# Kernel tuning notes

Hardware: AMD Instinct MI355X
Metric: run time of the kernel (lower is better)

Reference implementation:

```python
import jax, jax.numpy as jnp
import numpy as np

DELTA = 5.0          # weight on positive BCE term
R = 0.01             # hard-negative fraction
M, N = 4096, 16384   # batch rows, memory-bank size
NUM_HARD = int(R * (N - 1))  # int(r * neg_count); each row has exactly 1 positive


def setup_inputs() -> dict:
    key = jax.random.key(0)
    k1, k2 = jax.random.split(key)
    inputs = jax.random.normal(k1, (M, N), dtype=jnp.float32)
    targets = jax.random.randint(k2, (M,), 0, N)
    return {"inputs": inputs, "targets": targets}


def reference(inputs, targets):
    m, n = inputs.shape
    rows = jnp.arange(m)
    # positive logit per row (one-hot scatter => exactly one positive)
    pos = inputs[rows, targets]                          # [m]
    # BCE with logits, target=1: softplus(-x); mean over the single positive
    l_pos = jax.nn.softplus(-pos)                        # [m]
    # exclude positive from negatives by sinking it to -inf, then hard top-k
    neg_inf = jnp.finfo(inputs.dtype).min
    masked = inputs.at[rows, targets].set(neg_inf)       # [m, n]
    hard_neg, _ = jax.lax.top_k(masked, NUM_HARD)        # [m, NUM_HARD]
    # BCE with logits, target=0: softplus(x); mean over hard negatives
    l_neg = jnp.mean(jax.nn.softplus(hard_neg), axis=1)  # [m]
    return jnp.mean(DELTA * l_pos + l_neg)
```

## Files before the change

### kernel.cpp

```cpp
#include <hip/hip_runtime.h>
#include <stdint.h>

#define M_ROWS 4096
#define N_COLS 16384
#define K_HARD 163
#define DELTA_W 5.0f
#define CAPW   256
#define NWAVE  4
#define CAP    (CAPW * NWAVE)
#define NB     1024
#define BLOCK  256

#define KEY_MIN  0xC0000000u
#define BIN_BIAS 3072

__device__ __forceinline__ uint32_t f2key(float x) {
    uint32_t u = __float_as_uint(x);
    return u ^ (uint32_t)(((int32_t)u >> 31) | 0x80000000u);
}
__device__ __forceinline__ float key2f(uint32_t k) {
    uint32_t u = (k & 0x80000000u) ? (k & 0x7fffffffu) : ~k;
    return __uint_as_float(u);
}
__device__ __forceinline__ float softplus_f(float x) {
    return fmaxf(x, 0.0f) + log1pf(__expf(-fabsf(x)));
}

__device__ void pivot_scan(const uint32_t* hist, int K,
                           int* part, int* pivot, int* krem) {
    const int t = threadIdx.x;
    const int bpt = NB / BLOCK;
    const int base = t * bpt;
    int mypart = 0;
    for (int i = 0; i < bpt; ++i) mypart += (int)hist[base + i];
    part[t] = mypart;
    __syncthreads();
    for (int off = 1; off < BLOCK; off <<= 1) {
        int v = part[t];
        if (t + off < BLOCK) v += part[t + off];
        __syncthreads();
        part[t] = v;
        __syncthreads();
    }
    const int above = part[t] - mypart;
    if (above < K && above + mypart >= K) {
        int running = above;
        for (int b = base + bpt - 1; b >= base; --b) {
            int c = (int)hist[b];
            if (running < K && running + c >= K) { *pivot = b; *krem = K - running; }
            running += c;
        }
    }
    __syncthreads();
}

__global__ __launch_bounds__(BLOCK) void mmcl_kernel(
        const float* __restrict__ inputs,
        const int* __restrict__ targets,
        float* __restrict__ out) {
    __shared__ uint32_t s_hist[NB];
    __shared__ uint32_t s_cand[CAP];
    __shared__ uint32_t s_cand2[CAP];
    __shared__ int s_part[BLOCK];
    __shared__ int s_cnt[NWAVE];
    __shared__ int s_found;
    __shared__ int s_pivot;
    __shared__ int s_krem;
    __shared__ float s_wsum[NWAVE];

    const int row = blockIdx.x;
    const int t = threadIdx.x;
    const int lane = t & 63;
    const int wid = t >> 6;
    const float* rowp = inputs + (size_t)row * N_COLS;
    const int target = targets[row];

    for (int i = t; i < NB; i += BLOCK) s_hist[i] = 0;
    if (t == 0) s_found = -1;

    uint32_t* wcand = s_cand + wid * CAPW;
    int wcount = 0;
    const float4* rp4 = (const float4*)rowp;
#pragma unroll 4
    for (int it = 0; it < N_COLS / (BLOCK * 4); ++it) {
        const float4 v = rp4[it * BLOCK + t];
        const float vals[4] = {v.x, v.y, v.z, v.w};
#pragma unroll
        for (int c = 0; c < 4; ++c) {
            const uint32_t k = f2key(vals[c]);
            const bool pred = (k >= KEY_MIN);
            const unsigned long long mask = __ballot(pred);
            if (pred) {
                const int below = __builtin_amdgcn_mbcnt_hi(
                    (uint32_t)(mask >> 32),
                    __builtin_amdgcn_mbcnt_lo((uint32_t)mask, 0));
                const int off = wcount + below;
                if (off < CAPW) wcand[off] = k;
            }
            wcount += (int)__popcll(mask);
        }
    }
    if (lane == 0) s_cnt[wid] = wcount;
    __syncthreads();

    const int c0 = s_cnt[0], c1 = s_cnt[1], c2 = s_cnt[2], c3 = s_cnt[3];
    const int total = c0 + c1 + c2 + c3;
    const bool no_ovf = (c0 <= CAPW) & (c1 <= CAPW) & (c2 <= CAPW) & (c3 <= CAPW);
    const int wbase = (wid > 0 ? c0 : 0) + (wid > 1 ? c1 : 0) + (wid > 2 ? c2 : 0);

    const float pos = rowp[target];
    const uint32_t tkey = f2key(pos);

    if (no_ovf) {
        const int mycnt = s_cnt[wid];
        for (int i = lane; i < mycnt; i += 64) s_cand2[wbase + i] = wcand[i];
    }
    __syncthreads();

    if (no_ovf && tkey >= KEY_MIN) {
        for (int i = t; i < total; i += BLOCK)
            if (s_cand2[i] == tkey) { atomicCAS(&s_found, -1, i); break; }
    }
    __syncthreads();
    int ncand = total;
    if (s_found >= 0) {
        if (t == 0) s_cand2[s_found] = s_cand2[total - 1];
        ncand = total - 1;
    }
    __syncthreads();
    const bool fast = no_ovf && (ncand >= K_HARD);

    float local = 0.0f;
    uint32_t T;
    int tie;

    if (fast) {
        for (int i = t; i < ncand; i += BLOCK)
            atomicAdd(&s_hist[(s_cand2[i] >> 20) - BIN_BIAS], 1u);
        __syncthreads();
        pivot_scan(s_hist, K_HARD, s_part, &s_pivot, &s_krem);
        const int p1b = s_pivot + BIN_BIAS, k1r = s_krem;

        for (int i = t; i < NB; i += BLOCK) s_hist[i] = 0;
        __syncthreads();
        for (int i = t; i < ncand; i += BLOCK) {
            const uint32_t k = s_cand2[i];
            if ((int)(k >> 20) == p1b) atomicAdd(&s_hist[(k >> 10) & 1023u], 1u);
        }
        __syncthreads();
        pivot_scan(s_hist, k1r, s_part, &s_pivot, &s_krem);
        const int p2 = s_pivot, k2r = s_krem;
        const uint32_t pref2 = ((uint32_t)p1b << 10) | (uint32_t)p2;

        for (int i = t; i < NB; i += BLOCK) s_hist[i] = 0;
        __syncthreads();
        for (int i = t; i < ncand; i += BLOCK) {
            const uint32_t k = s_cand2[i];
            if ((k >> 10) == pref2) atomicAdd(&s_hist[k & 1023u], 1u);
        }
        __syncthreads();
        pivot_scan(s_hist, k2r, s_part, &s_pivot, &s_krem);
        T = (pref2 << 10) | (uint32_t)s_pivot;
        tie = s_krem;

        for (int i = t; i < ncand; i += BLOCK) {
            const uint32_t k = s_cand2[i];
            if (k > T) local += softplus_f(key2f(k));
        }
    } else {
        for (int i = t; i < NB; i += BLOCK) s_hist[i] = 0;
        __syncthreads();
        for (int j = t; j < N_COLS; j += BLOCK) {
            if (j == target) continue;
            atomicAdd(&s_hist[f2key(rowp[j]) >> 22], 1u);
        }
        __syncthreads();
        pivot_scan(s_hist, K_HARD, s_part, &s_pivot, &s_krem);
        const int p1 = s_pivot, k1r = s_krem;

        for (int i = t; i < NB; i += BLOCK) s_hist[i] = 0;
        __syncthreads();
        for (int j = t; j < N_COLS; j += BLOCK) {
            if (j == target) continue;
            const uint32_t k = f2key(rowp[j]);
            if ((int)(k >> 22) == p1) atomicAdd(&s_hist[(k >> 12) & 1023u], 1u);
        }
        __syncthreads();
        pivot_scan(s_hist, k1r, s_part, &s_pivot, &s_krem);
        const uint32_t pref2 = ((uint32_t)p1 << 10) | (uint32_t)s_pivot;
        const int k2r = s_krem;

        for (int i = t; i < NB; i += BLOCK) s_hist[i] = 0;
        __syncthreads();
        for (int j = t; j < N_COLS; j += BLOCK) {
            if (j == target) continue;
            const uint32_t k = f2key(rowp[j]);
            if ((k >> 12) == pref2) atomicAdd(&s_hist[(k >> 2) & 1023u], 1u);
        }
        __syncthreads();
        pivot_scan(s_hist, k2r, s_part, &s_pivot, &s_krem);
        const uint32_t pref3 = (pref2 << 10) | (uint32_t)s_pivot;
        const int k3r = s_krem;

        for (int i = t; i < NB; i += BLOCK) s_hist[i] = 0;
        __syncthreads();
        for (int j = t; j < N_COLS; j += BLOCK) {
            if (j == target) continue;
            const uint32_t k = f2key(rowp[j]);
            if ((k >> 2) == pref3) atomicAdd(&s_hist[k & 3u], 1u);
        }
        __syncthreads();
        if (t == 0) {
            int running = 0;
            for (int b = 3; b >= 0; --b) {
                const int c = (int)s_hist[b];
                if (running < k3r && running + c >= k3r) {
                    s_pivot = b; s_krem = k3r - running;
                }
                running += c;
            }
        }
        __syncthreads();
        T = (pref3 << 2) | (uint32_t)s_pivot;
        tie = s_krem;

        for (int j = t; j < N_COLS; j += BLOCK) {
            if (j == target) continue;
            const uint32_t k = f2key(rowp[j]);
            if (k > T) local += softplus_f(key2f(k));
        }
    }

    for (int off = 32; off > 0; off >>= 1) local += __shfl_down(local, off);
    if (lane == 0) s_wsum[wid] = local;
    __syncthreads();
    if (t == 0) {
        float tot = 0.0f;
        for (int w = 0; w < NWAVE; ++w) tot += s_wsum[w];
        tot += (float)tie * softplus_f(key2f(T));
        const float l_neg = tot / (float)K_HARD;
        const float l_pos = softplus_f(-pos);
        const float rowval = (DELTA_W * l_pos + l_neg) * (1.0f / (float)M_ROWS);
        atomicAdd(out, rowval);
    }
}

__global__ void mmcl_zero_out(float* out) { out[0] = 0.0f; }

extern "C" void kernel_launch(void* const* d_in, const int* in_sizes, int n_in,
                              void* d_out, int out_size, void* d_ws, size_t ws_size,
                              hipStream_t stream) {
    const float* inputs = (const float*)d_in[0];
    const int* targets = (const int*)d_in[1];
    float* out = (float*)d_out;
    mmcl_zero_out<<<1, 1, 0, stream>>>(out);
    mmcl_kernel<<<M_ROWS, BLOCK, 0, stream>>>(inputs, targets, out);
}
```

Baseline: 382.5 us.

## Replace ballot compaction and three-pass radix select with per-thread slots and one-pass histogram

Candidate collection drops the per-element wave ballot and compaction. Each thread now writes values at or above 2.0 into private shared-memory slots without branching, and a prefix scan compacts them into one array. Top-k selection replaces three histogram-plus-pivot passes with one 1024-bin histogram over the candidate range, a shuffle-based suffix scan, and an exact rank sort of the pivot bin's few elements. This cuts barriers and LDS atomics per row, at the cost of more shared memory, which may lower occupancy, and a full-row fallback when slots or the small buffer overflow.

```diff
diff --git a/kernel.cpp b/kernel.cpp
--- a/kernel.cpp
+++ b/kernel.cpp
@@ -5,14 +5,13 @@
 #define N_COLS 16384
 #define K_HARD 163
 #define DELTA_W 5.0f
-#define CAPW   256
-#define NWAVE  4
-#define CAP    (CAPW * NWAVE)
+#define BLOCK  256
+#define SLOTS  12
+#define CAP    1024
 #define NB     1024
-#define BLOCK  256
-
-#define KEY_MIN  0xC0000000u
-#define BIN_BIAS 3072
+#define SMALL  64
+#define THRESH 2.0f
+#define KEY_MIN 0xC0000000u
 
 __device__ __forceinline__ uint32_t f2key(float x) {
     uint32_t u = __float_as_uint(x);
@@ -58,15 +57,13 @@
         const float* __restrict__ inputs,
         const int* __restrict__ targets,
         float* __restrict__ out) {
-    __shared__ uint32_t s_hist[NB];
+    __shared__ float    s_slots_f[BLOCK * SLOTS];
     __shared__ uint32_t s_cand[CAP];
-    __shared__ uint32_t s_cand2[CAP];
-    __shared__ int s_part[BLOCK];
-    __shared__ int s_cnt[NWAVE];
-    __shared__ int s_found;
-    __shared__ int s_pivot;
-    __shared__ int s_krem;
-    __shared__ float s_wsum[NWAVE];
+    __shared__ int s_wt[4], s_wm[4];
+    __shared__ int s_found, s_pivot, s_krem, s_nsmall;
+    __shared__ uint32_t s_skey[SMALL];
+    __shared__ int s_sidx[SMALL];
+    __shared__ float s_fw[4];
 
     const int row = blockIdx.x;
     const int t = threadIdx.x;
@@ -75,145 +72,174 @@
     const float* rowp = inputs + (size_t)row * N_COLS;
     const int target = targets[row];
 
-    for (int i = t; i < NB; i += BLOCK) s_hist[i] = 0;
     if (t == 0) s_found = -1;
 
-    uint32_t* wcand = s_cand + wid * CAPW;
-    int wcount = 0;
+    float* myslots = s_slots_f + t * SLOTS;
+    uint32_t cnt = 0;
     const float4* rp4 = (const float4*)rowp;
 #pragma unroll 4
     for (int it = 0; it < N_COLS / (BLOCK * 4); ++it) {
         const float4 v = rp4[it * BLOCK + t];
-        const float vals[4] = {v.x, v.y, v.z, v.w};
-#pragma unroll
-        for (int c = 0; c < 4; ++c) {
-            const uint32_t k = f2key(vals[c]);
-            const bool pred = (k >= KEY_MIN);
-            const unsigned long long mask = __ballot(pred);
-            if (pred) {
-                const int below = __builtin_amdgcn_mbcnt_hi(
-                    (uint32_t)(mask >> 32),
-                    __builtin_amdgcn_mbcnt_lo((uint32_t)mask, 0));
-                const int off = wcount + below;
-                if (off < CAPW) wcand[off] = k;
-            }
-            wcount += (int)__popcll(mask);
-        }
-    }
-    if (lane == 0) s_cnt[wid] = wcount;
-    __syncthreads();
-
-    const int c0 = s_cnt[0], c1 = s_cnt[1], c2 = s_cnt[2], c3 = s_cnt[3];
-    const int total = c0 + c1 + c2 + c3;
-    const bool no_ovf = (c0 <= CAPW) & (c1 <= CAPW) & (c2 <= CAPW) & (c3 <= CAPW);
-    const int wbase = (wid > 0 ? c0 : 0) + (wid > 1 ? c1 : 0) + (wid > 2 ? c2 : 0);
+        myslots[min(cnt, (uint32_t)(SLOTS - 1))] = v.x; cnt += (v.x >= THRESH);
+        myslots[min(cnt, (uint32_t)(SLOTS - 1))] = v.y; cnt += (v.y >= THRESH);
+        myslots[min(cnt, (uint32_t)(SLOTS - 1))] = v.z; cnt += (v.z >= THRESH);
+        myslots[min(cnt, (uint32_t)(SLOTS - 1))] = v.w; cnt += (v.w >= THRESH);
+    }
+
+    const int stored = (int)min(cnt, (uint32_t)SLOTS);
+    int inc = stored;
+    for (int off = 1; off < 64; off <<= 1) {
+        int y = __shfl_up(inc, off);
+        if (lane >= off) inc += y;
+    }
+    int mx = (int)cnt;
+    for (int off = 1; off < 64; off <<= 1)
+        mx = max(mx, __shfl_xor(mx, off));
+    if (lane == 63) { s_wt[wid] = inc; }
+    if (lane == 0)  { s_wm[wid] = mx; }
+    __syncthreads();
+    const int w0 = s_wt[0], w1 = s_wt[1], w2 = s_wt[2], w3 = s_wt[3];
+    const int total = w0 + w1 + w2 + w3;
+    const int maxc = max(max(s_wm[0], s_wm[1]), max(s_wm[2], s_wm[3]));
+    const int wbase = (wid > 0 ? w0 : 0) + (wid > 1 ? w1 : 0) + (wid > 2 ? w2 : 0);
+    const int myoff = wbase + inc - stored;
+    for (int c = 0; c < stored; ++c) {
+        const int d = myoff + c;
+        if (d < CAP) s_cand[d] = f2key(myslots[c]);
+    }
+    __syncthreads();
 
     const float pos = rowp[target];
     const uint32_t tkey = f2key(pos);
-
-    if (no_ovf) {
-        const int mycnt = s_cnt[wid];
-        for (int i = lane; i < mycnt; i += 64) s_cand2[wbase + i] = wcand[i];
-    }
-    __syncthreads();
-
-    if (no_ovf && tkey >= KEY_MIN) {
-        for (int i = t; i < total; i += BLOCK)
-            if (s_cand2[i] == tkey) { atomicCAS(&s_found, -1, i); break; }
+    const int tclamp = min(total, CAP);
+    if (pos >= THRESH) {
+        for (int i = t; i < tclamp; i += BLOCK)
+            if (s_cand[i] == tkey) { atomicCAS(&s_found, -1, i); break; }
     }
     __syncthreads();
     int ncand = total;
     if (s_found >= 0) {
-        if (t == 0) s_cand2[s_found] = s_cand2[total - 1];
         ncand = total - 1;
-    }
-    __syncthreads();
-    const bool fast = no_ovf && (ncand >= K_HARD);
-
+        if (t == 0) s_cand[s_found] = s_cand[ncand];
+    }
+    __syncthreads();
+
+    const bool fast = (maxc <= SLOTS) && (total <= CAP) && (ncand >= K_HARD);
+    bool needfb = !fast;
     float local = 0.0f;
-    uint32_t T;
-    int tie;
+
+    uint32_t* hist = (uint32_t*)s_slots_f;
 
     if (fast) {
+        for (int i = t; i < NB; i += BLOCK) hist[i] = 0;
+        __syncthreads();
         for (int i = t; i < ncand; i += BLOCK)
-            atomicAdd(&s_hist[(s_cand2[i] >> 20) - BIN_BIAS], 1u);
-        __syncthreads();
-        pivot_scan(s_hist, K_HARD, s_part, &s_pivot, &s_krem);
-        const int p1b = s_pivot + BIN_BIAS, k1r = s_krem;
-
-        for (int i = t; i < NB; i += BLOCK) s_hist[i] = 0;
-        __syncthreads();
+            atomicAdd(&hist[min((s_cand[i] - KEY_MIN) >> 14, (uint32_t)(NB - 1))], 1u);
+        __syncthreads();
+
+        const int base4 = t * 4;
+        const int c0 = (int)hist[base4], c1 = (int)hist[base4 + 1],
+                  c2 = (int)hist[base4 + 2], c3 = (int)hist[base4 + 3];
+        const int own = c0 + c1 + c2 + c3;
+        int suf = own;
+        for (int off = 1; off < 64; off <<= 1) {
+            int y = __shfl_down(suf, off);
+            if (lane + off < 64) suf += y;
+        }
+        if (lane == 0) s_wt[wid] = suf;
+        if (t == 0) s_nsmall = 0;
+        __syncthreads();
+        int wsuf = 0;
+        for (int w = wid + 1; w < 4; ++w) wsuf += s_wt[w];
+        int run = wsuf + (suf - own);
+        {
+            const int cs[4] = {c0, c1, c2, c3};
+            for (int b = 3; b >= 0; --b) {
+                const int c = cs[b];
+                if (run < K_HARD && run + c >= K_HARD) {
+                    s_pivot = base4 + b; s_krem = K_HARD - run;
+                }
+                run += c;
+            }
+        }
+        __syncthreads();
+        const uint32_t B = (uint32_t)s_pivot;
+        const int krem = s_krem;
+
         for (int i = t; i < ncand; i += BLOCK) {
-            const uint32_t k = s_cand2[i];
-            if ((int)(k >> 20) == p1b) atomicAdd(&s_hist[(k >> 10) & 1023u], 1u);
-        }
-        __syncthreads();
-        pivot_scan(s_hist, k1r, s_part, &s_pivot, &s_krem);
-        const int p2 = s_pivot, k2r = s_krem;
-        const uint32_t pref2 = ((uint32_t)p1b << 10) | (uint32_t)p2;
-
-        for (int i = t; i < NB; i += BLOCK) s_hist[i] = 0;
-        __syncthreads();
-        for (int i = t; i < ncand; i += BLOCK) {
-            const uint32_t k = s_cand2[i];
-            if ((k >> 10) == pref2) atomicAdd(&s_hist[k & 1023u], 1u);
-        }
-        __syncthreads();
-        pivot_scan(s_hist, k2r, s_part, &s_pivot, &s_krem);
-        T = (pref2 << 10) | (uint32_t)s_pivot;
-        tie = s_krem;
-
-        for (int i = t; i < ncand; i += BLOCK) {
-            const uint32_t k = s_cand2[i];
-            if (k > T) local += softplus_f(key2f(k));
-        }
-    } else {
-        for (int i = t; i < NB; i += BLOCK) s_hist[i] = 0;
-        __syncthreads();
-        for (int j = t; j < N_COLS; j += BLOCK) {
-            if (j == target) continue;
-            atomicAdd(&s_hist[f2key(rowp[j]) >> 22], 1u);
-        }
-        __syncthreads();
-        pivot_scan(s_hist, K_HARD, s_part, &s_pivot, &s_krem);
+            const uint32_t k = s_cand[i];
+            const uint32_t kb = min((k - KEY_MIN) >> 14, (uint32_t)(NB - 1));
+            if (kb > B) local += softplus_f(key2f(k));
+            else if (kb == B) {
+                const int d = atomicAdd(&s_nsmall, 1);
+                if (d < SMALL) { s_skey[d] = k; s_sidx[d] = i; }
+            }
+        }
+        __syncthreads();
+        const int m = s_nsmall;
+        if (m > SMALL) { needfb = true; local = 0.0f; }
+        else {
+            for (int i = t; i < m; i += BLOCK) {
+                const uint32_t ki = s_skey[i]; const int ii = s_sidx[i];
+                int r = 0;
+                for (int j = 0; j < m; ++j) {
+                    const uint32_t kj = s_skey[j];
+                    r += (kj > ki) || (kj == ki && s_sidx[j] < ii);
+                }
+                if (r < krem) local += softplus_f(key2f(ki));
+            }
+        }
+    }
+
+    if (needfb) {
+        local = 0.0f;
+        int* part = (int*)s_cand;
+        for (int i = t; i < NB; i += BLOCK) hist[i] = 0;
+        __syncthreads();
+        for (int j = t; j < N_COLS; j += BLOCK) {
+            if (j == target) continue;
+            atomicAdd(&hist[f2key(rowp[j]) >> 22], 1u);
+        }
+        __syncthreads();
+        pivot_scan(hist, K_HARD, part, &s_pivot, &s_krem);
         const int p1 = s_pivot, k1r = s_krem;
 
-        for (int i = t; i < NB; i += BLOCK) s_hist[i] = 0;
-        __syncthreads();
-        for (int j = t; j < N_COLS; j += BLOCK) {
-            if (j == target) continue;
-            const uint32_t k = f2key(rowp[j]);
-            if ((int)(k >> 22) == p1) atomicAdd(&s_hist[(k >> 12) & 1023u], 1u);
-        }
-        __syncthreads();
-        pivot_scan(s_hist, k1r, s_part, &s_pivot, &s_krem);
+        for (int i = t; i < NB; i += BLOCK) hist[i] = 0;
+        __syncthreads();
+        for (int j = t; j < N_COLS; j += BLOCK) {
+            if (j == target) continue;
+            const uint32_t k = f2key(rowp[j]);
+            if ((int)(k >> 22) == p1) atomicAdd(&hist[(k >> 12) & 1023u], 1u);
+        }
+        __syncthreads();
+        pivot_scan(hist, k1r, part, &s_pivot, &s_krem);
         const uint32_t pref2 = ((uint32_t)p1 << 10) | (uint32_t)s_pivot;
         const int k2r = s_krem;
 
-        for (int i = t; i < NB; i += BLOCK) s_hist[i] = 0;
-        __syncthreads();
-        for (int j = t; j < N_COLS; j += BLOCK) {
-            if (j == target) continue;
-            const uint32_t k = f2key(rowp[j]);
-            if ((k >> 12) == pref2) atomicAdd(&s_hist[(k >> 2) & 1023u], 1u);
-        }
-        __syncthreads();
-        pivot_scan(s_hist, k2r, s_part, &s_pivot, &s_krem);
+        for (int i = t; i < NB; i += BLOCK) hist[i] = 0;
+        __syncthreads();
+        for (int j = t; j < N_COLS; j += BLOCK) {
+            if (j == target) continue;
+            const uint32_t k = f2key(rowp[j]);
+            if ((k >> 12) == pref2) atomicAdd(&hist[(k >> 2) & 1023u], 1u);
+        }
+        __syncthreads();
+        pivot_scan(hist, k2r, part, &s_pivot, &s_krem);
         const uint32_t pref3 = (pref2 << 10) | (uint32_t)s_pivot;
         const int k3r = s_krem;
 
-        for (int i = t; i < NB; i += BLOCK) s_hist[i] = 0;
-        __syncthreads();
-        for (int j = t; j < N_COLS; j += BLOCK) {
-            if (j == target) continue;
-            const uint32_t k = f2key(rowp[j]);
-            if ((k >> 2) == pref3) atomicAdd(&s_hist[k & 3u], 1u);
+        for (int i = t; i < 4; i += BLOCK) hist[i] = 0;
+        __syncthreads();
+        for (int j = t; j < N_COLS; j += BLOCK) {
+            if (j == target) continue;
+            const uint32_t k = f2key(rowp[j]);
+            if ((k >> 2) == pref3) atomicAdd(&hist[k & 3u], 1u);
         }
         __syncthreads();
         if (t == 0) {
             int running = 0;
             for (int b = 3; b >= 0; --b) {
-                const int c = (int)s_hist[b];
+                const int c = (int)hist[b];
                 if (running < k3r && running + c >= k3r) {
                     s_pivot = b; s_krem = k3r - running;
                 }
@@ -221,23 +247,22 @@
             }
         }
         __syncthreads();
-        T = (pref3 << 2) | (uint32_t)s_pivot;
-        tie = s_krem;
+        const uint32_t T = (pref3 << 2) | (uint32_t)s_pivot;
+        const int tie = s_krem;
 
         for (int j = t; j < N_COLS; j += BLOCK) {
             if (j == target) continue;
             const uint32_t k = f2key(rowp[j]);
             if (k > T) local += softplus_f(key2f(k));
         }
+        if (t == 0) local += (float)tie * softplus_f(key2f(T));
     }
 
     for (int off = 32; off > 0; off >>= 1) local += __shfl_down(local, off);
-    if (lane == 0) s_wsum[wid] = local;
+    if (lane == 0) s_fw[wid] = local;
     __syncthreads();
     if (t == 0) {
-        float tot = 0.0f;
-        for (int w = 0; w < NWAVE; ++w) tot += s_wsum[w];
-        tot += (float)tie * softplus_f(key2f(T));
+        const float tot = s_fw[0] + s_fw[1] + s_fw[2] + s_fw[3];
         const float l_neg = tot / (float)K_HARD;
         const float l_pos = softplus_f(-pos);
         const float rowval = (DELTA_W * l_pos + l_neg) * (1.0f / (float)M_ROWS);
```

After: 359.7 us. -6.0%, faster.
